# Performance work log

Hardware: AMD Instinct MI355X
Metric: run time of the kernel (lower is better)

Reference implementation:

```python
import jax, jax.numpy as jnp
import numpy as np
from jax import lax


def _conv(x, w, b, pad, groups):
    # NCHW conv, kernel OIHW, stride 1, symmetric padding, grouped.
    y = lax.conv_general_dilated(
        x, w, window_strides=(1, 1), padding=[(pad, pad), (pad, pad)],
        dimension_numbers=("NCHW", "OIHW", "NCHW"), feature_group_count=groups)
    return y if b is None else y + b[None, :, None, None]


def setup_inputs() -> dict:
    key = jax.random.key(0)
    ks = jax.random.split(key, 8)
    B, C, H, W = 8, 128, 128, 128
    nh = 8
    c3 = C * 3            # pos conv output channels
    o = (C // 2) * 3      # each QKV dconv output channels (3C/2)
    ch = C // 2           # SSA dconv output channels
    s = 0.05
    return {
        "x": jax.random.normal(ks[0], (B, C, H, W), jnp.float32),
        "pos_w": jax.random.normal(ks[1], (c3, C, 1, 1), jnp.float32) * s,
        "pos_b": jnp.zeros((c3,), jnp.float32),
        "qd3_w": jax.random.normal(ks[2], (o, 2, 3, 3), jnp.float32) * s,
        "qd3_b": jnp.zeros((o,), jnp.float32),
        "qd5_w": jax.random.normal(ks[3], (o, 2, 5, 5), jnp.float32) * s,
        "qd5_b": jnp.zeros((o,), jnp.float32),
        "temp": jnp.ones((nh, 1, 1), jnp.float32),
        "d3_w": jax.random.normal(ks[4], (ch, 2, 3, 3), jnp.float32) * s,
        "d3_b": jnp.zeros((ch,), jnp.float32),
        "d5_w": jax.random.normal(ks[5], (ch, 2, 5, 5), jnp.float32) * s,
        "d5_b": jnp.zeros((ch,), jnp.float32),
        "proj_w": jax.random.normal(ks[6], (C, 2 * C, 1, 1), jnp.float32) * s,
        "num_head": 8,
    }


def _l2norm(a):
    # F.normalize(dim=-1): x / max(||x||, 1e-12)
    n = jnp.sqrt(jnp.sum(a * a, axis=-1, keepdims=True))
    return a / jnp.maximum(n, 1e-12)


def reference(x, pos_w, pos_b, qd3_w, qd3_b, qd5_w, qd5_b, temp,
              d3_w, d3_b, d5_w, d5_b, proj_w, num_head):
    B, C, H, W = x.shape
    hw = H * W
    # QKV module: 1x1 pos conv -> two grouped dconvs (groups = out channels = 3C/2) -> concat
    t = _conv(x, pos_w, pos_b, 0, 1)                      # (B, 3C, H, W)
    g = qd3_w.shape[0]                                     # 3C/2 groups
    qkv = jnp.concatenate(
        (_conv(t, qd3_w, qd3_b, 1, g), _conv(t, qd5_w, qd5_b, 2, g)), axis=1)  # (B, 3C, H, W)
    qkv = qkv.reshape(B, 3, num_head, -1, hw)              # (B, 3, nh, d, hw)
    q, k, v = qkv[:, 0], qkv[:, 1], qkv[:, 2]
    q = _l2norm(q)
    k = _l2norm(k)
    # transposed (channel) attention: d x d per head, temperature-scaled softmax
    attn = jax.nn.softmax(jnp.einsum("bhdn,bhen->bhde", q, k) * temp[None], axis=-1)
    out = jnp.einsum("bhde,bhen->bhdn", attn, v).reshape(B, C, H, W)
    ch = C // 2
    y = jnp.concatenate(
        (out, _conv(x, d3_w, d3_b, 1, ch), _conv(x, d5_w, d5_b, 2, ch)), axis=1)  # (B, 2C, H, W)
    return _conv(y, proj_w, None, 0, 1)                    # 1x1 proj, no bias
```

## Files before the change

kernel.cpp:

```cpp
#include <hip/hip_runtime.h>
#include <hip/hip_bf16.h>


#define HW 16384
#define HH 128
#define WW 128

typedef __attribute__((ext_vector_type(8))) short bf16x8;
typedef __attribute__((ext_vector_type(8))) _Float16 f16x8;
typedef __attribute__((ext_vector_type(4))) float f32x4;
typedef __attribute__((ext_vector_type(4))) unsigned short us4;
typedef _Float16 half2t __attribute__((ext_vector_type(2)));

__device__ inline unsigned short f2bf(float f) {
    unsigned u = __float_as_uint(f);
    return (unsigned short)((u + 0x7FFFu + ((u >> 16) & 1u)) >> 16);
}
__device__ inline float bf2f(unsigned short us) {
    return __uint_as_float(((unsigned)us) << 16);
}
__device__ inline unsigned packbf(float lo, float hi) {
    return (unsigned)f2bf(lo) | ((unsigned)f2bf(hi) << 16);
}
__device__ inline unsigned short f2h(float f) {
    _Float16 h = (_Float16)f;
    return __builtin_bit_cast(unsigned short, h);
}
__device__ inline unsigned packh(float lo, float hi) {
    return (unsigned)f2h(lo) | ((unsigned)f2h(hi) << 16);
}

#if defined(__has_builtin)
#if __has_builtin(__builtin_amdgcn_fdot2)
#define HAVE_FDOT2 1
#endif
#endif

__device__ inline float dot2acc(unsigned a, unsigned b, float c) {
#ifdef HAVE_FDOT2
    return __builtin_amdgcn_fdot2(__builtin_bit_cast(half2t, a),
                                  __builtin_bit_cast(half2t, b), c, false);
#else
    half2t ha = __builtin_bit_cast(half2t, a);
    half2t hb = __builtin_bit_cast(half2t, b);
    return c + (float)ha[0] * (float)hb[0] + (float)ha[1] * (float)hb[1];
#endif
}

__global__ void zerok(float* p, int n) {
    int i = blockIdx.x * 256 + threadIdx.x;
    if (i < n) p[i] = 0.f;
}

__global__ __launch_bounds__(256) void packx(const float* __restrict__ x,
                                             unsigned* __restrict__ xpk, int nb) {
    long id = (long)blockIdx.x * 256 + threadIdx.x;
    if (id >= (long)nb * 64 * (HW / 4)) return;
    int n4 = (int)(id % (HW / 4));
    long rest = id / (HW / 4);
    int p = (int)(rest & 63);
    int b = (int)(rest >> 6);
    const float* r0 = x + ((long)b * 128 + 2 * p) * HW + n4 * 4;
    float4 a = *(const float4*)r0;
    float4 c = *(const float4*)(r0 + HW);
    uint4 o;
    o.x = packh(a.x, c.x); o.y = packh(a.y, c.y);
    o.z = packh(a.z, c.z); o.w = packh(a.w, c.w);
    *(uint4*)(xpk + ((long)b * 64 + p) * HW + n4 * 4) = o;
}

__global__ __launch_bounds__(256) void packw(const float* __restrict__ w,
                                             unsigned* __restrict__ wpk) {
    int id = blockIdx.x * 256 + threadIdx.x;
    if (id >= 384 * 64) return;
    int m = id >> 6, kp = id & 63;
    wpk[id] = packh(w[m * 128 + 2 * kp], w[m * 128 + 2 * kp + 1]);
}

__global__ __launch_bounds__(256) void packcw(
    const float* __restrict__ qd3, const float* __restrict__ qd5,
    const float* __restrict__ d3, const float* __restrict__ d5,
    unsigned* __restrict__ o) {
    int id = blockIdx.x * 256 + threadIdx.x;
    if (id < 192 * 9) {
        int g = id / 9, tp = id % 9;
        o[id] = packh(qd3[(g * 2) * 9 + tp], qd3[(g * 2 + 1) * 9 + tp]);
    } else if (id < 192 * 9 + 192 * 25) {
        int r = id - 192 * 9; int g = r / 25, tp = r % 25;
        o[id] = packh(qd5[(g * 2) * 25 + tp], qd5[(g * 2 + 1) * 25 + tp]);
    } else if (id < 192 * 9 + 192 * 25 + 64 * 9) {
        int r = id - 192 * 9 - 192 * 25; int g = r / 9, tp = r % 9;
        o[id] = packh(d3[(g * 2) * 9 + tp], d3[(g * 2 + 1) * 9 + tp]);
    } else if (id < 192 * 9 + 192 * 25 + 64 * 9 + 64 * 25) {
        int r = id - 192 * 9 - 192 * 25 - 64 * 9; int g = r / 25, tp = r % 25;
        o[id] = packh(d5[(g * 2) * 25 + tp], d5[(g * 2 + 1) * 25 + tp]);
    }
}

__global__ __launch_bounds__(256) void gemm_t(
    const unsigned* __restrict__ wpk,
    const unsigned* __restrict__ xpk,
    const float* __restrict__ posb,
    unsigned* __restrict__ tpk)
{
    int b = blockIdx.z;
    int n0 = blockIdx.x * 64;
    const unsigned* xb = xpk + (long)b * 64 * HW;
    unsigned* tb = tpk + (long)b * 192 * HW;
    __shared__ unsigned Bs[64][65];
    int tid = threadIdx.x;
    {
        int kp = tid >> 2, nq = tid & 3;
        const unsigned* src = xb + (long)kp * HW + n0 + nq * 16;
        uint4 v0 = *(const uint4*)(src);
        uint4 v1 = *(const uint4*)(src + 4);
        uint4 v2 = *(const uint4*)(src + 8);
        uint4 v3 = *(const uint4*)(src + 12);
        int nb_ = nq * 16;
        Bs[nb_ + 0][kp] = v0.x;  Bs[nb_ + 1][kp] = v0.y;
        Bs[nb_ + 2][kp] = v0.z;  Bs[nb_ + 3][kp] = v0.w;
        Bs[nb_ + 4][kp] = v1.x;  Bs[nb_ + 5][kp] = v1.y;
        Bs[nb_ + 6][kp] = v1.z;  Bs[nb_ + 7][kp] = v1.w;
        Bs[nb_ + 8][kp] = v2.x;  Bs[nb_ + 9][kp] = v2.y;
        Bs[nb_ + 10][kp] = v2.z; Bs[nb_ + 11][kp] = v2.w;
        Bs[nb_ + 12][kp] = v3.x; Bs[nb_ + 13][kp] = v3.y;
        Bs[nb_ + 14][kp] = v3.z; Bs[nb_ + 15][kp] = v3.w;
    }
    __syncthreads();
    int w = tid >> 6, l = tid & 63;
    int lr = l & 15, lg = l >> 4;
    f32x4 acc[6][4] = {};
    #pragma unroll
    for (int kk = 0; kk < 4; ++kk) {
        f16x8 af[6];
        #pragma unroll
        for (int mt = 0; mt < 6; ++mt) {
            int m = (w * 6 + mt) * 16 + lr;
            af[mt] = *(const f16x8*)(wpk + (long)m * 64 + kk * 16 + lg * 4);
        }
        #pragma unroll
        for (int ns = 0; ns < 4; ++ns) {
            f16x8 bf = *(const f16x8*)(&Bs[ns * 16 + lr][kk * 16 + lg * 4]);
            #pragma unroll
            for (int mt = 0; mt < 6; ++mt)
                acc[mt][ns] = __builtin_amdgcn_mfma_f32_16x16x32_f16(
                    af[mt], bf, acc[mt][ns], 0, 0, 0);
        }
    }
    #pragma unroll
    for (int mt = 0; mt < 6; ++mt) {
        int m0 = w * 96 + mt * 16 + lg * 4;
        float b0v = posb[m0], b1v = posb[m0 + 1], b2v = posb[m0 + 2], b3v = posb[m0 + 3];
        int p0 = m0 >> 1;
        #pragma unroll
        for (int ns = 0; ns < 4; ++ns) {
            int col = n0 + ns * 16 + lr;
            tb[(long)p0 * HW + col]       = packh(acc[mt][ns][0] + b0v, acc[mt][ns][1] + b1v);
            tb[(long)(p0 + 1) * HW + col] = packh(acc[mt][ns][2] + b2v, acc[mt][ns][3] + b3v);
        }
    }
}

__global__ __launch_bounds__(256) void dualconv(
    const unsigned* __restrict__ src, int srcP,
    const unsigned* __restrict__ w3pk, const float* __restrict__ b3,
    const unsigned* __restrict__ w5pk, const float* __restrict__ b5,
    int s3, unsigned short* __restrict__ r3a, long st3a,
    unsigned short* __restrict__ r3b, long st3b,
    int s5, unsigned short* __restrict__ r5a, long st5a,
    unsigned short* __restrict__ r5b, long st5b)
{
    int gp = blockIdx.y, b = blockIdx.z, y0 = blockIdx.x * 8;
    __shared__ __align__(16) unsigned tile[2][12][132];
    int tid = threadIdx.x;
    const unsigned* sb = src + ((long)b * srcP + 2 * gp) * HW;
    const int TOT = 2 * 12 * 132;
    for (int idx = tid; idx < TOT; idx += 256) {
        int gi = idx / (12 * 132);
        int rem = idx - gi * (12 * 132);
        int r = rem / 132, ci = rem - r * 132;
        int row = y0 + r - 2, col = ci - 2;
        unsigned u = 0;
        if (row >= 0 && row < HH && col >= 0 && col < WW)
            u = sb[(long)gi * HW + row * WW + col];
        tile[gi][r][ci] = u;
    }
    __syncthreads();
    int xq = tid & 31, yy = tid >> 5;
    int x0 = xq * 4;
    float a3[2][4], a5[2][4];
    #pragma unroll
    for (int gi = 0; gi < 2; ++gi) {
        int g = 2 * gp + gi;
        #pragma unroll
        for (int j = 0; j < 4; ++j) { a3[gi][j] = b3[g]; a5[gi][j] = b5[g]; }
        unsigned w5v[25], w3v[9];
        #pragma unroll
        for (int i = 0; i < 25; ++i) w5v[i] = w5pk[g * 25 + i];
        #pragma unroll
        for (int i = 0; i < 9; ++i) w3v[i] = w3pk[g * 9 + i];
        #pragma unroll
        for (int r = 0; r < 5; ++r) {
            const unsigned* p = &tile[gi][yy + r][x0];
            unsigned win[8];
            *(f32x4*)win = *(const f32x4*)p;
            *(f32x4*)(win + 4) = *(const f32x4*)(p + 4);
            #pragma unroll
            for (int dx = 0; dx < 5; ++dx)
                #pragma unroll
                for (int j = 0; j < 4; ++j)
                    a5[gi][j] = dot2acc(win[j + dx], w5v[r * 5 + dx], a5[gi][j]);
            if (r >= 1 && r <= 3) {
                #pragma unroll
                for (int dx = 0; dx < 3; ++dx)
                    #pragma unroll
                    for (int j = 0; j < 4; ++j)
                        a3[gi][j] = dot2acc(win[j + dx + 1], w3v[(r - 1) * 3 + dx], a3[gi][j]);
            }
        }
    }
    long prow = (long)(y0 + yy) * WW + x0;
    #pragma unroll
    for (int gi = 0; gi < 2; ++gi) {
        int g = 2 * gp + gi;
        us4 v3, v5;
        #pragma unroll
        for (int j = 0; j < 4; ++j) { v3[j] = f2bf(a3[gi][j]); v5[j] = f2bf(a5[gi][j]); }
        unsigned short* d3 = (g < s3) ? r3a + (long)b * st3a + (long)g * HW
                                      : r3b + (long)b * st3b + (long)(g - s3) * HW;
        unsigned short* d5 = (g < s5) ? r5a + (long)b * st5a + (long)g * HW
                                      : r5b + (long)b * st5b + (long)(g - s5) * HW;
        *(us4*)(d3 + prow) = v3;
        *(us4*)(d5 + prow) = v5;
    }
}

__global__ __launch_bounds__(64) void gram_mfma(
    const unsigned short* __restrict__ q,
    const unsigned short* __restrict__ k,
    float* __restrict__ gbuf)
{
    int bh = blockIdx.x, chunk = blockIdx.y;
    int b = bh >> 3, h = bh & 7;
    int l = threadIdx.x;
    int r = l & 15, koff = (l >> 4) * 8;
    const unsigned short* qrow = q + ((long)b * 128 + h * 16 + r) * HW;
    const unsigned short* krow = k + ((long)b * 128 + h * 16 + r) * HW;
    f32x4 acc = {0.f, 0.f, 0.f, 0.f};
    float sq = 0.f, sk = 0.f;
    int n0 = chunk * 512;
    for (int n = n0; n < n0 + 512; n += 32) {
        bf16x8 af = *(const bf16x8*)(qrow + n + koff);
        bf16x8 bf = *(const bf16x8*)(krow + n + koff);
        #pragma unroll
        for (int j = 0; j < 8; ++j) {
            float fq = bf2f((unsigned short)af[j]);
            float fk = bf2f((unsigned short)bf[j]);
            sq += fq * fq; sk += fk * fk;
        }
        acc = __builtin_amdgcn_mfma_f32_16x16x32_bf16(af, bf, acc, 0, 0, 0);
    }
    float* gb = gbuf + bh * 288;
    #pragma unroll
    for (int reg = 0; reg < 4; ++reg) {
        int row = (l >> 4) * 4 + reg;
        atomicAdd(&gb[row * 16 + r], acc[reg]);
    }
    sq += __shfl_xor(sq, 16); sq += __shfl_xor(sq, 32);
    sk += __shfl_xor(sk, 16); sk += __shfl_xor(sk, 32);
    if (l < 16) { atomicAdd(&gb[256 + r], sq); atomicAdd(&gb[272 + r], sk); }
}

__global__ __launch_bounds__(256) void attn_fold(
    const float* __restrict__ gbuf, const float* __restrict__ temp,
    const float* __restrict__ projw,
    unsigned* __restrict__ wallpk)
{
    int bh = blockIdx.x;
    int b = bh >> 3, h = bh & 7;
    const float* gb = gbuf + bh * 288;
    __shared__ float logit[16][16];
    __shared__ float A[16][16];
    int tid = threadIdx.x;
    int d = tid >> 4, e = tid & 15;
    {
        float nq = fmaxf(sqrtf(gb[256 + d]), 1e-12f);
        float nk = fmaxf(sqrtf(gb[272 + e]), 1e-12f);
        logit[d][e] = gb[d * 16 + e] / (nq * nk) * temp[h];
    }
    __syncthreads();
    float m = -1e30f;
    #pragma unroll
    for (int j = 0; j < 16; ++j) m = fmaxf(m, logit[d][j]);
    float ex = expf(logit[d][e] - m);
    A[d][e] = ex;
    __syncthreads();
    float sum = 0.f;
    #pragma unroll
    for (int j = 0; j < 16; ++j) sum += A[d][j];
    __syncthreads();
    A[d][e] = ex / sum;
    __syncthreads();
    int ep = tid & 7, co0 = tid >> 3;
    for (int co = co0; co < 128; co += 32) {
        float lo = 0.f, hi = 0.f;
        #pragma unroll
        for (int dd = 0; dd < 16; ++dd) {
            float pw = projw[co * 256 + h * 16 + dd];
            lo += pw * A[dd][2 * ep];
            hi += pw * A[dd][2 * ep + 1];
        }
        wallpk[((long)b * 128 + co) * 128 + h * 8 + ep] = packbf(lo, hi);
    }
    if (h == 0) {
        for (int idx = tid; idx < 128 * 64; idx += 256) {
            int co = idx >> 6, cp = idx & 63;
            wallpk[((long)b * 128 + co) * 128 + 64 + cp] =
                packbf(projw[co * 256 + 128 + 2 * cp], projw[co * 256 + 129 + 2 * cp]);
        }
    }
}

__global__ __launch_bounds__(256) void gemm_out(
    const unsigned* __restrict__ wpk,
    const unsigned short* __restrict__ vy,
    float* __restrict__ out)
{
    int b = blockIdx.z;
    int n0 = blockIdx.x * 32;
    const unsigned* wb = wpk + (long)b * 128 * 128;
    const unsigned short* vyb = vy + (long)b * 256 * HW;
    float* ob = out + (long)b * 128 * HW;
    __shared__ unsigned Bs[32][129];
    int tid = threadIdx.x;
    int oct = tid & 7, kpb = tid >> 3;
    #pragma unroll
    for (int p = 0; p < 4; ++p) {
        int kp = p * 32 + kpb;
        us4 lo = *(const us4*)(vyb + (long)(2 * kp) * HW + n0 + oct * 4);
        us4 hi = *(const us4*)(vyb + (long)(2 * kp + 1) * HW + n0 + oct * 4);
        #pragma unroll
        for (int j = 0; j < 4; ++j)
            Bs[oct * 4 + j][kp] = (unsigned)lo[j] | ((unsigned)hi[j] << 16);
    }
    __syncthreads();
    int w = tid >> 6, l = tid & 63;
    int lr = l & 15, lg = l >> 4;
    f32x4 acc[2][2] = {};
    #pragma unroll
    for (int kk = 0; kk < 8; ++kk) {
        bf16x8 af[2];
        #pragma unroll
        for (int i = 0; i < 2; ++i) {
            int m = (w * 2 + i) * 16 + lr;
            af[i] = *(const bf16x8*)(wb + (long)m * 128 + kk * 16 + lg * 4);
        }
        #pragma unroll
        for (int ns = 0; ns < 2; ++ns) {
            bf16x8 bf = *(const bf16x8*)(&Bs[ns * 16 + lr][kk * 16 + lg * 4]);
            #pragma unroll
            for (int i = 0; i < 2; ++i)
                acc[i][ns] = __builtin_amdgcn_mfma_f32_16x16x32_bf16(
                    af[i], bf, acc[i][ns], 0, 0, 0);
        }
    }
    #pragma unroll
    for (int i = 0; i < 2; ++i)
        #pragma unroll
        for (int ns = 0; ns < 2; ++ns)
            #pragma unroll
            for (int reg = 0; reg < 4; ++reg) {
                int m = (w * 2 + i) * 16 + lg * 4 + reg;
                ob[(long)m * HW + n0 + ns * 16 + lr] = acc[i][ns][reg];
            }
}

extern "C" void kernel_launch(void* const* d_in, const int* in_sizes, int n_in,
                              void* d_out, int out_size, void* d_ws, size_t ws_size,
                              hipStream_t stream) {
    const float* x      = (const float*)d_in[0];
    const float* pos_w  = (const float*)d_in[1];
    const float* pos_b  = (const float*)d_in[2];
    const float* qd3_w  = (const float*)d_in[3];
    const float* qd3_b  = (const float*)d_in[4];
    const float* qd5_w  = (const float*)d_in[5];
    const float* qd5_b  = (const float*)d_in[6];
    const float* temp   = (const float*)d_in[7];
    const float* d3_w   = (const float*)d_in[8];
    const float* d3_b   = (const float*)d_in[9];
    const float* d5_w   = (const float*)d_in[10];
    const float* d5_b   = (const float*)d_in[11];
    const float* proj_w = (const float*)d_in[12];
    float* out = (float*)d_out;

    size_t perb = (size_t)HW * 1792 + 65536;
    size_t fixedb = 64UL * 288 * 4 + 384UL * 64 * 4 + 8704UL * 4;
    int NB = 8;
    while (NB > 1 && (size_t)NB * perb + fixedb > ws_size) NB >>= 1;

    char* base = (char*)d_ws;
    unsigned* tpk      = (unsigned*)base;       base += (size_t)NB * 192 * HW * 4;
    unsigned* xpk      = (unsigned*)base;
    unsigned short* qb = (unsigned short*)base; base += (size_t)NB * 128 * HW * 2;
    unsigned short* kb = (unsigned short*)base; base += (size_t)NB * 128 * HW * 2;
    unsigned short* vy = (unsigned short*)base; base += (size_t)NB * 256 * HW * 2;
    unsigned* wallpk   = (unsigned*)base;       base += (size_t)NB * 128 * 128 * 4;
    float* gram        = (float*)base;          base += 64UL * 288 * 4;
    unsigned* poswpk   = (unsigned*)base;       base += 384UL * 64 * 4;
    unsigned* cwpk     = (unsigned*)base;
    unsigned* qd3pk = cwpk;
    unsigned* qd5pk = cwpk + 192 * 9;
    unsigned* d3pk  = cwpk + 192 * 9 + 192 * 25;
    unsigned* d5pk  = cwpk + 192 * 9 + 192 * 25 + 64 * 9;

    packw<<<(384 * 64 + 255) / 256, 256, 0, stream>>>(pos_w, poswpk);
    packcw<<<(8704 + 255) / 256, 256, 0, stream>>>(qd3_w, qd5_w, d3_w, d5_w, cwpk);

    for (int b0 = 0; b0 < 8; b0 += NB) {
        const float* xb = x + (long)b0 * 128 * HW;
        float* outb = out + (long)b0 * 128 * HW;

        packx<<<NB * 1024, 256, 0, stream>>>(xb, xpk, NB);

        gemm_t<<<dim3(HW / 64, 1, NB), 256, 0, stream>>>(poswpk, xpk, pos_b, tpk);

        dualconv<<<dim3(16, 32, NB), 256, 0, stream>>>(
            xpk, 64, d3pk, d3_b, d5pk, d5_b,
            64, vy + 128L * HW, 256L * HW, vy + 128L * HW, 256L * HW,
            64, vy + 192L * HW, 256L * HW, vy + 192L * HW, 256L * HW);

        dualconv<<<dim3(16, 96, NB), 256, 0, stream>>>(
            tpk, 192, qd3pk, qd3_b, qd5pk, qd5_b,
            128, qb, 128L * HW, kb, 128L * HW,
            64, kb + 64L * HW, 128L * HW, vy, 256L * HW);

        zerok<<<(64 * 288 + 255) / 256, 256, 0, stream>>>(gram, 64 * 288);
        gram_mfma<<<dim3(NB * 8, 32), 64, 0, stream>>>(qb, kb, gram);
        attn_fold<<<NB * 8, 256, 0, stream>>>(gram, temp, proj_w, wallpk);

        gemm_out<<<dim3(HW / 32, 1, NB), 256, 0, stream>>>(wallpk, vy, outb);
    }
}
```

Before: 238.4 us.

## Fuse x packing into consumers, compute norms via MFMA, widen output GEMM tile

Removes the separate packx kernel. gemm_t and the x-side dualconv now read fp32 x directly and convert it to packed fp16 on the fly, which drops a full write and re-read of the packed intermediate. dualconv gets a templated row-wise tile loader, and gram_mfma computes the squared norms with extra MFMAs (q·q, k·k diagonals) in place of scalar bf16 unpacking. gemm_out doubles its N tile to 64 with wider vector loads, at the cost of more registers and LDS per block.

Result: slower. 254.8 us (+6.9%).

```diff
diff --git a/kernel.cpp b/kernel.cpp
--- a/kernel.cpp
+++ b/kernel.cpp
@@ -15,9 +15,6 @@
 __device__ inline unsigned short f2bf(float f) {
     unsigned u = __float_as_uint(f);
     return (unsigned short)((u + 0x7FFFu + ((u >> 16) & 1u)) >> 16);
-}
-__device__ inline float bf2f(unsigned short us) {
-    return __uint_as_float(((unsigned)us) << 16);
 }
 __device__ inline unsigned packbf(float lo, float hi) {
     return (unsigned)f2bf(lo) | ((unsigned)f2bf(hi) << 16);
@@ -50,23 +47,6 @@
 __global__ void zerok(float* p, int n) {
     int i = blockIdx.x * 256 + threadIdx.x;
     if (i < n) p[i] = 0.f;
-}
-
-__global__ __launch_bounds__(256) void packx(const float* __restrict__ x,
-                                             unsigned* __restrict__ xpk, int nb) {
-    long id = (long)blockIdx.x * 256 + threadIdx.x;
-    if (id >= (long)nb * 64 * (HW / 4)) return;
-    int n4 = (int)(id % (HW / 4));
-    long rest = id / (HW / 4);
-    int p = (int)(rest & 63);
-    int b = (int)(rest >> 6);
-    const float* r0 = x + ((long)b * 128 + 2 * p) * HW + n4 * 4;
-    float4 a = *(const float4*)r0;
-    float4 c = *(const float4*)(r0 + HW);
-    uint4 o;
-    o.x = packh(a.x, c.x); o.y = packh(a.y, c.y);
-    o.z = packh(a.z, c.z); o.w = packh(a.w, c.w);
-    *(uint4*)(xpk + ((long)b * 64 + p) * HW + n4 * 4) = o;
 }
 
 __global__ __launch_bounds__(256) void packw(const float* __restrict__ w,
@@ -99,32 +79,30 @@
 
 __global__ __launch_bounds__(256) void gemm_t(
     const unsigned* __restrict__ wpk,
-    const unsigned* __restrict__ xpk,
+    const float* __restrict__ x,
     const float* __restrict__ posb,
     unsigned* __restrict__ tpk)
 {
     int b = blockIdx.z;
     int n0 = blockIdx.x * 64;
-    const unsigned* xb = xpk + (long)b * 64 * HW;
+    const float* xb = x + (long)b * 128 * HW;
     unsigned* tb = tpk + (long)b * 192 * HW;
     __shared__ unsigned Bs[64][65];
     int tid = threadIdx.x;
     {
         int kp = tid >> 2, nq = tid & 3;
-        const unsigned* src = xb + (long)kp * HW + n0 + nq * 16;
-        uint4 v0 = *(const uint4*)(src);
-        uint4 v1 = *(const uint4*)(src + 4);
-        uint4 v2 = *(const uint4*)(src + 8);
-        uint4 v3 = *(const uint4*)(src + 12);
+        const float* s0 = xb + (long)(2 * kp) * HW + n0 + nq * 16;
+        const float* s1 = s0 + HW;
         int nb_ = nq * 16;
-        Bs[nb_ + 0][kp] = v0.x;  Bs[nb_ + 1][kp] = v0.y;
-        Bs[nb_ + 2][kp] = v0.z;  Bs[nb_ + 3][kp] = v0.w;
-        Bs[nb_ + 4][kp] = v1.x;  Bs[nb_ + 5][kp] = v1.y;
-        Bs[nb_ + 6][kp] = v1.z;  Bs[nb_ + 7][kp] = v1.w;
-        Bs[nb_ + 8][kp] = v2.x;  Bs[nb_ + 9][kp] = v2.y;
-        Bs[nb_ + 10][kp] = v2.z; Bs[nb_ + 11][kp] = v2.w;
-        Bs[nb_ + 12][kp] = v3.x; Bs[nb_ + 13][kp] = v3.y;
-        Bs[nb_ + 14][kp] = v3.z; Bs[nb_ + 15][kp] = v3.w;
+        #pragma unroll
+        for (int q4 = 0; q4 < 4; ++q4) {
+            float4 lo = *(const float4*)(s0 + q4 * 4);
+            float4 hi = *(const float4*)(s1 + q4 * 4);
+            Bs[nb_ + q4 * 4 + 0][kp] = packh(lo.x, hi.x);
+            Bs[nb_ + q4 * 4 + 1][kp] = packh(lo.y, hi.y);
+            Bs[nb_ + q4 * 4 + 2][kp] = packh(lo.z, hi.z);
+            Bs[nb_ + q4 * 4 + 3][kp] = packh(lo.w, hi.w);
+        }
     }
     __syncthreads();
     int w = tid >> 6, l = tid & 63;
@@ -161,8 +139,9 @@
     }
 }
 
+template<bool PK>
 __global__ __launch_bounds__(256) void dualconv(
-    const unsigned* __restrict__ src, int srcP,
+    const void* __restrict__ src_, int srcCP,
     const unsigned* __restrict__ w3pk, const float* __restrict__ b3,
     const unsigned* __restrict__ w5pk, const float* __restrict__ b5,
     int s3, unsigned short* __restrict__ r3a, long st3a,
@@ -173,17 +152,31 @@
     int gp = blockIdx.y, b = blockIdx.z, y0 = blockIdx.x * 8;
     __shared__ __align__(16) unsigned tile[2][12][132];
     int tid = threadIdx.x;
-    const unsigned* sb = src + ((long)b * srcP + 2 * gp) * HW;
-    const int TOT = 2 * 12 * 132;
-    for (int idx = tid; idx < TOT; idx += 256) {
-        int gi = idx / (12 * 132);
-        int rem = idx - gi * (12 * 132);
-        int r = rem / 132, ci = rem - r * 132;
-        int row = y0 + r - 2, col = ci - 2;
-        unsigned u = 0;
-        if (row >= 0 && row < HH && col >= 0 && col < WW)
-            u = sb[(long)gi * HW + row * WW + col];
-        tile[gi][r][ci] = u;
+    int giF = tid >> 7, lane = tid & 127;
+    const unsigned* sU = (const unsigned*)src_ + ((long)b * srcCP + 2 * gp + giF) * HW;
+    const float* sF = (const float*)src_ + ((long)b * srcCP + 4 * gp + 2 * giF) * HW;
+    #pragma unroll
+    for (int r = 0; r < 12; ++r) {
+        int row = y0 + r - 2;
+        bool rok = (unsigned)row < (unsigned)HH;
+        {
+            int col = lane - 2;
+            unsigned u = 0;
+            if (rok && (unsigned)col < (unsigned)WW) {
+                long o = (long)row * WW + col;
+                u = PK ? sU[o] : packh(sF[o], sF[o + HW]);
+            }
+            tile[giF][r][lane] = u;
+        }
+        if (lane < 4) {
+            int col = 126 + lane;
+            unsigned u = 0;
+            if (rok && col < WW) {
+                long o = (long)row * WW + col;
+                u = PK ? sU[o] : packh(sF[o], sF[o + HW]);
+            }
+            tile[giF][r][128 + lane] = u;
+        }
     }
     __syncthreads();
     int xq = tid & 31, yy = tid >> 5;
@@ -223,15 +216,17 @@
     #pragma unroll
     for (int gi = 0; gi < 2; ++gi) {
         int g = 2 * gp + gi;
-        us4 v3, v5;
-        #pragma unroll
-        for (int j = 0; j < 4; ++j) { v3[j] = f2bf(a3[gi][j]); v5[j] = f2bf(a5[gi][j]); }
+        uint2 v3, v5;
+        v3.x = packbf(a3[gi][0], a3[gi][1]);
+        v3.y = packbf(a3[gi][2], a3[gi][3]);
+        v5.x = packbf(a5[gi][0], a5[gi][1]);
+        v5.y = packbf(a5[gi][2], a5[gi][3]);
         unsigned short* d3 = (g < s3) ? r3a + (long)b * st3a + (long)g * HW
                                       : r3b + (long)b * st3b + (long)(g - s3) * HW;
         unsigned short* d5 = (g < s5) ? r5a + (long)b * st5a + (long)g * HW
                                       : r5b + (long)b * st5b + (long)(g - s5) * HW;
-        *(us4*)(d3 + prow) = v3;
-        *(us4*)(d5 + prow) = v5;
+        *(uint2*)(d3 + prow) = v3;
+        *(uint2*)(d5 + prow) = v5;
     }
 }
 
@@ -246,29 +241,27 @@
     int r = l & 15, koff = (l >> 4) * 8;
     const unsigned short* qrow = q + ((long)b * 128 + h * 16 + r) * HW;
     const unsigned short* krow = k + ((long)b * 128 + h * 16 + r) * HW;
-    f32x4 acc = {0.f, 0.f, 0.f, 0.f};
-    float sq = 0.f, sk = 0.f;
+    f32x4 accS = {0.f, 0.f, 0.f, 0.f};
+    f32x4 accQ = {0.f, 0.f, 0.f, 0.f};
+    f32x4 accK = {0.f, 0.f, 0.f, 0.f};
     int n0 = chunk * 512;
     for (int n = n0; n < n0 + 512; n += 32) {
         bf16x8 af = *(const bf16x8*)(qrow + n + koff);
         bf16x8 bf = *(const bf16x8*)(krow + n + koff);
-        #pragma unroll
-        for (int j = 0; j < 8; ++j) {
-            float fq = bf2f((unsigned short)af[j]);
-            float fk = bf2f((unsigned short)bf[j]);
-            sq += fq * fq; sk += fk * fk;
-        }
-        acc = __builtin_amdgcn_mfma_f32_16x16x32_bf16(af, bf, acc, 0, 0, 0);
+        accS = __builtin_amdgcn_mfma_f32_16x16x32_bf16(af, bf, accS, 0, 0, 0);
+        accQ = __builtin_amdgcn_mfma_f32_16x16x32_bf16(af, af, accQ, 0, 0, 0);
+        accK = __builtin_amdgcn_mfma_f32_16x16x32_bf16(bf, bf, accK, 0, 0, 0);
     }
     float* gb = gbuf + bh * 288;
     #pragma unroll
     for (int reg = 0; reg < 4; ++reg) {
         int row = (l >> 4) * 4 + reg;
-        atomicAdd(&gb[row * 16 + r], acc[reg]);
-    }
-    sq += __shfl_xor(sq, 16); sq += __shfl_xor(sq, 32);
-    sk += __shfl_xor(sk, 16); sk += __shfl_xor(sk, 32);
-    if (l < 16) { atomicAdd(&gb[256 + r], sq); atomicAdd(&gb[272 + r], sk); }
+        atomicAdd(&gb[row * 16 + r], accS[reg]);
+        if (row == r) {
+            atomicAdd(&gb[256 + r], accQ[reg]);
+            atomicAdd(&gb[272 + r], accK[reg]);
+        }
+    }
 }
 
 __global__ __launch_bounds__(256) void attn_fold(
@@ -327,26 +320,33 @@
     float* __restrict__ out)
 {
     int b = blockIdx.z;
-    int n0 = blockIdx.x * 32;
+    int n0 = blockIdx.x * 64;
     const unsigned* wb = wpk + (long)b * 128 * 128;
     const unsigned short* vyb = vy + (long)b * 256 * HW;
     float* ob = out + (long)b * 128 * HW;
-    __shared__ unsigned Bs[32][129];
+    __shared__ unsigned Bs[64][129];
     int tid = threadIdx.x;
-    int oct = tid & 7, kpb = tid >> 3;
-    #pragma unroll
-    for (int p = 0; p < 4; ++p) {
-        int kp = p * 32 + kpb;
-        us4 lo = *(const us4*)(vyb + (long)(2 * kp) * HW + n0 + oct * 4);
-        us4 hi = *(const us4*)(vyb + (long)(2 * kp + 1) * HW + n0 + oct * 4);
-        #pragma unroll
-        for (int j = 0; j < 4; ++j)
-            Bs[oct * 4 + j][kp] = (unsigned)lo[j] | ((unsigned)hi[j] << 16);
+    {
+        int kp = tid >> 1, nh = (tid & 1) * 32;
+        const unsigned short* s0 = vyb + (long)(2 * kp) * HW + n0 + nh;
+        const unsigned short* s1 = s0 + HW;
+        #pragma unroll
+        for (int q4 = 0; q4 < 4; ++q4) {
+            us4 lo0 = *(const us4*)(s0 + q4 * 8);
+            us4 lo1 = *(const us4*)(s0 + q4 * 8 + 4);
+            us4 hi0 = *(const us4*)(s1 + q4 * 8);
+            us4 hi1 = *(const us4*)(s1 + q4 * 8 + 4);
+            #pragma unroll
+            for (int j = 0; j < 4; ++j) {
+                Bs[nh + q4 * 8 + j][kp]     = (unsigned)lo0[j] | ((unsigned)hi0[j] << 16);
+                Bs[nh + q4 * 8 + 4 + j][kp] = (unsigned)lo1[j] | ((unsigned)hi1[j] << 16);
+            }
+        }
     }
     __syncthreads();
     int w = tid >> 6, l = tid & 63;
     int lr = l & 15, lg = l >> 4;
-    f32x4 acc[2][2] = {};
+    f32x4 acc[2][4] = {};
     #pragma unroll
     for (int kk = 0; kk < 8; ++kk) {
         bf16x8 af[2];
@@ -356,7 +356,7 @@
             af[i] = *(const bf16x8*)(wb + (long)m * 128 + kk * 16 + lg * 4);
         }
         #pragma unroll
-        for (int ns = 0; ns < 2; ++ns) {
+        for (int ns = 0; ns < 4; ++ns) {
             bf16x8 bf = *(const bf16x8*)(&Bs[ns * 16 + lr][kk * 16 + lg * 4]);
             #pragma unroll
             for (int i = 0; i < 2; ++i)
@@ -367,7 +367,7 @@
     #pragma unroll
     for (int i = 0; i < 2; ++i)
         #pragma unroll
-        for (int ns = 0; ns < 2; ++ns)
+        for (int ns = 0; ns < 4; ++ns)
             #pragma unroll
             for (int reg = 0; reg < 4; ++reg) {
                 int m = (w * 2 + i) * 16 + lg * 4 + reg;
@@ -400,7 +400,6 @@
 
     char* base = (char*)d_ws;
     unsigned* tpk      = (unsigned*)base;       base += (size_t)NB * 192 * HW * 4;
-    unsigned* xpk      = (unsigned*)base;
     unsigned short* qb = (unsigned short*)base; base += (size_t)NB * 128 * HW * 2;
     unsigned short* kb = (unsigned short*)base; base += (size_t)NB * 128 * HW * 2;
     unsigned short* vy = (unsigned short*)base; base += (size_t)NB * 256 * HW * 2;
@@ -420,16 +419,14 @@
         const float* xb = x + (long)b0 * 128 * HW;
         float* outb = out + (long)b0 * 128 * HW;
 
-        packx<<<NB * 1024, 256, 0, stream>>>(xb, xpk, NB);
-
-        gemm_t<<<dim3(HW / 64, 1, NB), 256, 0, stream>>>(poswpk, xpk, pos_b, tpk);
-
-        dualconv<<<dim3(16, 32, NB), 256, 0, stream>>>(
-            xpk, 64, d3pk, d3_b, d5pk, d5_b,
+        gemm_t<<<dim3(HW / 64, 1, NB), 256, 0, stream>>>(poswpk, xb, pos_b, tpk);
+
+        dualconv<false><<<dim3(16, 32, NB), 256, 0, stream>>>(
+            xb, 128, d3pk, d3_b, d5pk, d5_b,
             64, vy + 128L * HW, 256L * HW, vy + 128L * HW, 256L * HW,
             64, vy + 192L * HW, 256L * HW, vy + 192L * HW, 256L * HW);
 
-        dualconv<<<dim3(16, 96, NB), 256, 0, stream>>>(
+        dualconv<true><<<dim3(16, 96, NB), 256, 0, stream>>>(
             tpk, 192, qd3pk, qd3_b, qd5pk, qd5_b,
             128, qb, 128L * HW, kb, 128L * HW,
             64, kb + 64L * HW, 128L * HW, vy, 256L * HW);
@@ -438,6 +435,6 @@
         gram_mfma<<<dim3(NB * 8, 32), 64, 0, stream>>>(qb, kb, gram);
         attn_fold<<<NB * 8, 256, 0, stream>>>(gram, temp, proj_w, wallpk);
 
-        gemm_out<<<dim3(HW / 32, 1, NB), 256, 0, stream>>>(wallpk, vy, outb);
-    }
-}
+        gemm_out<<<dim3(HW / 64, 1, NB), 256, 0, stream>>>(wallpk, vy, outb);
+    }
+}
```
